# Kernel tuning notes

Hardware: AMD Instinct MI355X
Metric: run time of the kernel (lower is better)

## Reference

```python
import jax, jax.numpy as jnp
import numpy as np

D, NH, NKV, HD, FF, V, T, GEN = 4096, 32, 8, 128, 14336, 1024, 32, 8
ROPE_THETA = 500000.0
EPS = 1e-5


def rms_norm(x, w):
    var = jnp.mean(jnp.square(x), axis=-1, keepdims=True)
    return (x * jax.lax.rsqrt(var + EPS)) * w


def rope_tables(max_pos):
    inv = 1.0 / (ROPE_THETA ** (jnp.arange(0, HD, 2, dtype=jnp.float32) / HD))
    freqs = jnp.arange(max_pos, dtype=jnp.float32)[:, None] * inv[None, :]  # [P, HD/2]
    emb = jnp.concatenate([freqs, freqs], axis=-1)  # [P, HD]
    return jnp.cos(emb), jnp.sin(emb)


def rotate_half(x):
    h = x.shape[-1] // 2
    return jnp.concatenate([-x[..., h:], x[..., :h]], axis=-1)


def setup_inputs() -> dict:
    key = jax.random.key(0)
    ks = jax.random.split(key, 16)
    s = 0.02
    return {
        "chunk_hidden_states": jax.random.normal(ks[0], (1, T, D), jnp.float32),
        "Wq": jax.random.normal(ks[1], (NH * HD, D), jnp.float32) * s,
        "Wk": jax.random.normal(ks[2], (NKV * HD, D), jnp.float32) * s,
        "Wv": jax.random.normal(ks[3], (NKV * HD, D), jnp.float32) * s,
        "Wo": jax.random.normal(ks[4], (D, NH * HD), jnp.float32) * s,
        "w_ln1": jnp.ones((D,), jnp.float32),
        "w_ln2": jnp.ones((D,), jnp.float32),
        "Wg": jax.random.normal(ks[5], (FF, D), jnp.float32) * s,
        "Wu": jax.random.normal(ks[6], (FF, D), jnp.float32) * s,
        "Wd": jax.random.normal(ks[7], (D, FF), jnp.float32) * s,
        "w_norm": jnp.ones((D,), jnp.float32),
        "emb": jax.random.normal(ks[8], (V, D), jnp.float32) * s,
        "W_out": jax.random.normal(ks[9], (V, D), jnp.float32) * s,
        "b_out": jnp.zeros((V,), jnp.float32),
    }


def reference(chunk_hidden_states, Wq, Wk, Wv, Wo, w_ln1, w_ln2, Wg, Wu, Wd,
              w_norm, emb, W_out, b_out):
    # inference=True path: for each of T time steps (processed in parallel here,
    # tokens, re-running the single Llama decoder layer on the growing sequence
    # each step (no KV cache). Only the LAST position's layer output feeds the
    # output head, so we compute q only for the last valid position, which is
    # mathematically identical to the original full-forward + [:, -1, :].
    G = NH // NKV  # query heads per kv head
    x0 = chunk_hidden_states[0]  # [T, D]
    buf = jnp.zeros((T, GEN + 1, D), jnp.float32).at[:, 0].set(x0)
    cos, sin = rope_tables(GEN + 1)  # [GEN+1, HD]
    scale = 1.0 / jnp.sqrt(jnp.float32(HD))

    def step(p, carry):
        buf, toks = carry
        h = rms_norm(buf, w_ln1)  # [T, S, D], S = GEN+1
        k = (h @ Wk.T).reshape(T, GEN + 1, NKV, HD)
        v = (h @ Wv.T).reshape(T, GEN + 1, NKV, HD)
        k = k * cos[None, :, None, :] + rotate_half(k) * sin[None, :, None, :]
        hq = jnp.take(h, p, axis=1)  # [T, D] last valid position
        q = (hq @ Wq.T).reshape(T, NH, HD)
        q = q * cos[p] + rotate_half(q) * sin[p]
        qg = q.reshape(T, NKV, G, HD)
        # scores over keys j (invalid / future keys masked; causal query is pos p)
        scores = jnp.einsum('tgcd,tjgd->tgcj', qg, k) * scale  # [T,NKV,G,S]
        valid = jnp.arange(GEN + 1) <= p
        scores = jnp.where(valid[None, None, None, :], scores, -jnp.inf)
        attn = jax.nn.softmax(scores, axis=-1)
        ao = jnp.einsum('tgcj,tjgd->tgcd', attn, v).reshape(T, NH * HD) @ Wo.T
        xp = jnp.take(buf, p, axis=1) + ao  # attention residual
        h2 = rms_norm(xp, w_ln2)
        mlp = (jax.nn.silu(h2 @ Wg.T) * (h2 @ Wu.T)) @ Wd.T
        xo = xp + mlp  # MLP residual; NOTE: no final norm in inference path
        logits = xo @ W_out.T + b_out  # [T, V]
        tok = jnp.argmax(logits, axis=-1)  # argmax(softmax) == argmax(logits)
        toks = toks.at[:, p].set(tok)
        buf = buf.at[:, p + 1].set(emb[tok])
        return buf, toks

    _, toks = jax.lax.fori_loop(0, GEN, step, (buf, jnp.zeros((T, GEN), jnp.int32)))
    return toks  # [T, 8] predicted tokens
```

## Files before the change

### kernel.cpp

```cpp
#include <hip/hip_runtime.h>
#include <hip/hip_bf16.h>

#define D 4096
#define NH 32
#define NKV 8
#define HD 128
#define FF 14336
#define VOC 1024
#define TT 32
#define GENN 8
#define SEQ 9

#define NQKV 6144
#define NGU  28672

#define OFF_BUF   0ull
#define OFF_KC    1179648ull
#define OFF_VC    1474560ull
#define OFF_AOT   1769472ull
#define OFF_XP    1900544ull
#define OFF_R1    2031616ull
#define OFF_R2    2031680ull
#define OFF_XPK   2031744ull
#define OFF_PART  2490496ull
#define OFF_RED   6684800ull
#define OFF_LR    6881408ull

typedef __attribute__((ext_vector_type(8))) short short8;
typedef __attribute__((ext_vector_type(16))) float f32x16;
typedef __attribute__((address_space(1))) void gv_t;
typedef __attribute__((address_space(3))) void lv_t;

__device__ inline void cvt_hi_lo(const float* x, short8& hi, short8& lo) {
    union U { unsigned u[4]; short8 s; };
    U H, L;
    #pragma unroll
    for (int j = 0; j < 4; ++j) {
        float2 p = make_float2(x[2 * j], x[2 * j + 1]);
        __hip_bfloat162 h = __float22bfloat162_rn(p);
        unsigned hb; __builtin_memcpy(&hb, &h, 4);
        H.u[j] = hb;
        float f0 = __uint_as_float(hb << 16);
        float f1 = __uint_as_float(hb & 0xffff0000u);
        __hip_bfloat162 l = __float22bfloat162_rn(make_float2(p.x - f0, p.y - f1));
        unsigned lb; __builtin_memcpy(&lb, &l, 4);
        L.u[j] = lb;
    }
    hi = H.s; lo = L.s;
}

__device__ inline void store_frag(unsigned* Xp, int frag, int lane,
                                  const short8& hi, const short8& lo) {
    unsigned* dst = Xp + (size_t)frag * 512 + lane * 4;
    union U { short8 s; uint4 u; };
    U uh, ul; uh.s = hi; ul.s = lo;
    *(uint4*)dst = uh.u;
    *(uint4*)(dst + 256) = ul.u;
}

__global__ void k_init(const float* __restrict__ x0, float* __restrict__ buf,
                       float* __restrict__ r1) {
    int t = blockIdx.x;
    const float* src = x0 + (size_t)t * D;
    float* dst = buf + (size_t)t * SEQ * D;
    float ss = 0.f;
    for (int d = threadIdx.x; d < D; d += 256) { float v = src[d]; dst[d] = v; ss += v * v; }
    #pragma unroll
    for (int m = 1; m < 64; m <<= 1) ss += __shfl_xor(ss, m);
    __shared__ float red[4];
    if ((threadIdx.x & 63) == 0) red[threadIdx.x >> 6] = ss;
    __syncthreads();
    if (threadIdx.x == 0) {
        float tot = red[0] + red[1] + red[2] + red[3];
        r1[t] = 1.0f / sqrtf(tot / (float)D + 1e-5f);
    }
}

__global__ void k_rms_rows(const float* __restrict__ x, float* __restrict__ r) {
    int t = blockIdx.x;
    const float* row = x + (size_t)t * D;
    float ss = 0.f;
    for (int d = threadIdx.x; d < D; d += 256) { float v = row[d]; ss += v * v; }
    #pragma unroll
    for (int m = 1; m < 64; m <<= 1) ss += __shfl_xor(ss, m);
    __shared__ float red[4];
    if ((threadIdx.x & 63) == 0) red[threadIdx.x >> 6] = ss;
    __syncthreads();
    if (threadIdx.x == 0) {
        float tot = red[0] + red[1] + red[2] + red[3];
        r[t] = 1.0f / sqrtf(tot / (float)D + 1e-5f);
    }
}

__global__ __launch_bounds__(256) void k_pack_norm(const float* __restrict__ src0,
        int rowStride, const float* __restrict__ r, const float* __restrict__ w,
        unsigned* __restrict__ Xp) {
    int frag = blockIdx.x * 4 + (threadIdx.x >> 6);
    int lane = threadIdx.x & 63;
    int m = lane & 31, half = lane >> 5;
    int k0 = frag * 16 + half * 8;
    const float* src = src0 + (size_t)m * rowStride + k0;
    float rr = r[m];
    float x[8];
    #pragma unroll
    for (int e = 0; e < 8; ++e) x[e] = src[e] * rr * w[k0 + e];
    short8 hi, lo; cvt_hi_lo(x, hi, lo); store_frag(Xp, frag, lane, hi, lo);
}

__global__ __launch_bounds__(256) void k_pack(const float* __restrict__ XT,
                                              unsigned* __restrict__ Xp) {
    int frag = blockIdx.x * 4 + (threadIdx.x >> 6);
    int lane = threadIdx.x & 63;
    int m = lane & 31, half = lane >> 5;
    const float* src = XT + (size_t)(frag * 16 + half * 8) * TT + m;
    float x[8];
    #pragma unroll
    for (int e = 0; e < 8; ++e) x[e] = src[e * TT];
    short8 hi, lo; cvt_hi_lo(x, hi, lo); store_frag(Xp, frag, lane, hi, lo);
}

__global__ __launch_bounds__(256, 2) void k_gemm3(
        const unsigned* __restrict__ Xp, const float* __restrict__ W0,
        const float* __restrict__ W1, const float* __restrict__ W2,
        int t1, int t2, float* __restrict__ part,
        int Nfull, int K, int ntiles, int kc) {
    __shared__ char smem[3 * 20480];
    int wave = threadIdx.x >> 6, lane = threadIdx.x & 63;
    int tile = blockIdx.x % ntiles, split = blockIdx.x / ntiles;
    int k0 = split * kc;
    int m = lane & 31, half = lane >> 5;
    const float* Wsel; int rt;
    if (tile < t1)      { Wsel = W0; rt = tile; }
    else if (tile < t2) { Wsel = W1; rt = tile - t1; }
    else                { Wsel = W2; rt = tile - t2; }
    int r8 = lane >> 3;
    int s8 = lane & 7;
    const float* wsrc = Wsel + (size_t)(rt * 128 + wave * 32 + r8) * K + k0 + ((s8 ^ r8) << 2);
    const unsigned* xsrc = Xp + ((size_t)(k0 >> 4) + (wave >> 1)) * 512 + (wave & 1) * 256 + lane * 4;
    int nph = kc >> 5;

    auto stagef = [&](int ph) {
        char* buf = smem + (ph % 3) * 20480;
        const float* wsp = wsrc + (size_t)ph * 32;
        char* wdb = buf + wave * 4096;
        #pragma unroll
        for (int q = 0; q < 4; ++q) {
            __builtin_amdgcn_global_load_lds(
                (gv_t*)(wsp + (size_t)(q * 8) * K),
                (lv_t*)(wdb + q * 1024), 16, 0, 0);
        }
        __builtin_amdgcn_global_load_lds(
            (gv_t*)(xsrc + (size_t)ph * 1024),
            (lv_t*)(buf + 16384 + wave * 1024), 16, 0, 0);
    };

    f32x16 acc;
    #pragma unroll
    for (int i = 0; i < 16; ++i) acc[i] = 0.f;

    stagef(0);
    if (nph > 1) stagef(1);
    union U { uint4 u; short8 s; };
    for (int ph = 0; ph < nph; ++ph) {
        if (ph + 1 < nph) { asm volatile("s_waitcnt vmcnt(5)" ::: "memory"); }
        else              { asm volatile("s_waitcnt vmcnt(0)" ::: "memory"); }
        __builtin_amdgcn_sched_barrier(0);
        __syncthreads();
        const char* buf = smem + (ph % 3) * 20480;
        const char* wrow = buf + (wave * 32 + m) * 128;
        const char* xb = buf + 16384;
        #pragma unroll
        for (int st = 0; st < 2; ++st) {
            int t0 = st * 4 + half * 2;
            float4 wa = *(const float4*)(wrow + ((t0 ^ (m & 7)) << 4));
            float4 wb = *(const float4*)(wrow + (((t0 + 1) ^ (m & 7)) << 4));
            float xv[8] = {wa.x, wa.y, wa.z, wa.w, wb.x, wb.y, wb.z, wb.w};
            short8 whi, wlo;
            cvt_hi_lo(xv, whi, wlo);
            U bh, bl;
            bh.u = *(const uint4*)(xb + st * 2048 + lane * 16);
            bl.u = *(const uint4*)(xb + st * 2048 + 1024 + lane * 16);
            acc = __builtin_amdgcn_mfma_f32_32x32x16_bf16(whi, bh.s, acc, 0, 0, 0);
            acc = __builtin_amdgcn_mfma_f32_32x32x16_bf16(whi, bl.s, acc, 0, 0, 0);
            acc = __builtin_amdgcn_mfma_f32_32x32x16_bf16(wlo, bh.s, acc, 0, 0, 0);
        }
        if (ph + 2 < nph) stagef(ph + 2);
    }
    int n0 = tile * 128 + wave * 32;
    float* dst = part + (size_t)split * Nfull * TT + (size_t)n0 * TT + m;
    #pragma unroll
    for (int r = 0; r < 16; ++r) {
        int rr = (r & 3) + 8 * (r >> 2) + 4 * half;
        dst[(size_t)rr * TT] = acc[r];
    }
}

__global__ void k_reduce_qkv(const float* __restrict__ part, float* __restrict__ red,
                             int S) {
    int idx = blockIdx.x * 256 + threadIdx.x;
    float a = 0.f;
    for (int s = 0; s < S; ++s) a += part[(size_t)s * NQKV * TT + idx];
    red[idx] = a;
}

__global__ __launch_bounds__(64) void k_attn_f(const float* __restrict__ red,
        float* __restrict__ kcache, float* __restrict__ vcache,
        float* __restrict__ aoT, int p) {
    int t = blockIdx.x >> 5, h = blockIdx.x & 31, kvh = h >> 2;
    int d = threadIdx.x;
    float a  = red[(size_t)(h * HD + d) * TT + t];
    float b  = red[(size_t)(h * HD + d + 64) * TT + t];
    float ak = red[(size_t)(4096 + kvh * HD + d) * TT + t];
    float bk = red[(size_t)(4096 + kvh * HD + d + 64) * TT + t];
    float v0 = red[(size_t)(5120 + kvh * HD + d) * TT + t];
    float v1 = red[(size_t)(5120 + kvh * HD + d + 64) * TT + t];
    float fp = (float)p;
    float ang = fp * powf(500000.0f, -(float)d * (1.0f / 64.0f));
    float cs = cosf(ang), sn = sinf(ang);
    float q0 = a * cs - b * sn,  q1 = b * cs + a * sn;
    float k0r = ak * cs - bk * sn, k1r = bk * cs + ak * sn;
    if ((h & 3) == 0) {
        float* krow = kcache + (((size_t)t * SEQ + p) * NKV + kvh) * HD;
        krow[d] = k0r; krow[d + 64] = k1r;
        float* vrow = vcache + (((size_t)t * SEQ + p) * NKV + kvh) * HD;
        vrow[d] = v0; vrow[d + 64] = v1;
    }
    const float scale = 0.08838834764831845f;
    float sc[SEQ];
    float mx = -1e30f;
    #pragma unroll
    for (int j = 0; j < SEQ; ++j) {
        int jj = (j < p) ? j : p;
        float k0j, k1j;
        if (jj == p) { k0j = k0r; k1j = k1r; }
        else {
            const float* kr = kcache + (((size_t)t * SEQ + jj) * NKV + kvh) * HD;
            k0j = kr[d]; k1j = kr[d + 64];
        }
        float ps = q0 * k0j + q1 * k1j;
        #pragma unroll
        for (int mm = 1; mm < 64; mm <<= 1) ps += __shfl_xor(ps, mm);
        ps = (j <= p) ? ps * scale : -1e30f;
        sc[j] = ps;
        mx = fmaxf(mx, ps);
    }
    float denom = 0.f;
    #pragma unroll
    for (int j = 0; j < SEQ; ++j) {
        float e = expf(sc[j] - mx);
        e = (j <= p) ? e : 0.f;
        sc[j] = e; denom += e;
    }
    float inv = 1.0f / denom;
    float o0 = 0.f, o1 = 0.f;
    #pragma unroll
    for (int j = 0; j < SEQ; ++j) {
        int jj = (j < p) ? j : p;
        float vv0, vv1;
        if (jj == p) { vv0 = v0; vv1 = v1; }
        else {
            const float* vr = vcache + (((size_t)t * SEQ + jj) * NKV + kvh) * HD;
            vv0 = vr[d]; vv1 = vr[d + 64];
        }
        float w = sc[j] * inv;
        o0 = fmaf(w, vv0, o0);
        o1 = fmaf(w, vv1, o1);
    }
    aoT[(size_t)(h * HD + d) * TT + t] = o0;
    aoT[(size_t)(h * HD + d + 64) * TT + t] = o1;
}

__global__ void k_reduce_o(const float* __restrict__ part, const float* __restrict__ buf,
                           float* __restrict__ xp, int p, int S) {
    int idx = blockIdx.x * 256 + threadIdx.x;
    int n = idx >> 5, t = idx & 31;
    float a = 0.f;
    for (int s = 0; s < S; ++s) a += part[(size_t)s * D * TT + idx];
    xp[(size_t)t * D + n] = a + buf[((size_t)t * SEQ + p) * D + n];
}

__global__ __launch_bounds__(256) void k_silu_pack(const float* __restrict__ part,
        unsigned* __restrict__ Xp, int S) {
    int frag = blockIdx.x * 4 + (threadIdx.x >> 6);
    int lane = threadIdx.x & 63;
    int m = lane & 31, half = lane >> 5;
    int n0 = frag * 16 + half * 8;
    float x[8];
    #pragma unroll
    for (int e = 0; e < 8; ++e) {
        int n = n0 + e;
        float g = 0.f, u = 0.f;
        for (int s = 0; s < S; ++s) {
            const float* pb = part + (size_t)s * NGU * TT;
            g += pb[(size_t)n * TT + m];
            u += pb[(size_t)(n + FF) * TT + m];
        }
        float sg = g / (1.0f + expf(-g));
        x[e] = sg * u;
    }
    short8 hi, lo; cvt_hi_lo(x, hi, lo); store_frag(Xp, frag, lane, hi, lo);
}

__global__ __launch_bounds__(256) void k_reduced_pack(const float* __restrict__ part,
        const float* __restrict__ xp, unsigned* __restrict__ Xp, int S) {
    int frag = blockIdx.x * 4 + (threadIdx.x >> 6);
    int lane = threadIdx.x & 63;
    int m = lane & 31, half = lane >> 5;
    int n0 = frag * 16 + half * 8;
    float x[8];
    #pragma unroll
    for (int e = 0; e < 8; ++e) {
        int n = n0 + e;
        float a = 0.f;
        for (int s = 0; s < S; ++s)
            a += part[(size_t)s * D * TT + (size_t)n * TT + m];
        x[e] = a + xp[(size_t)m * D + n];
    }
    short8 hi, lo; cvt_hi_lo(x, hi, lo); store_frag(Xp, frag, lane, hi, lo);
}

__global__ void k_logits_reduce(const float* __restrict__ part,
                                const float* __restrict__ bias,
                                float* __restrict__ lr, int S) {
    int idx = blockIdx.x * 256 + threadIdx.x;
    int n = idx >> 5;
    float a = bias[n];
    for (int s = 0; s < S; ++s) a += part[(size_t)s * VOC * TT + idx];
    lr[idx] = a;
}

__global__ void k_head(const float* __restrict__ lr, const float* __restrict__ emb,
                       int* __restrict__ toks, float* __restrict__ buf,
                       float* __restrict__ r1, int p) {
    int t = blockIdx.x;
    int tid = threadIdx.x;
    float bv = -1e30f; int bi = 0;
    for (int n = tid; n < VOC; n += 256) {
        float a = lr[(size_t)n * TT + t];
        if (a > bv) { bv = a; bi = n; }
    }
    __shared__ float sv[256];
    __shared__ int si[256];
    sv[tid] = bv; si[tid] = bi;
    __syncthreads();
    for (int off = 128; off > 0; off >>= 1) {
        if (tid < off) {
            float v2 = sv[tid + off]; int i2 = si[tid + off];
            if (v2 > sv[tid] || (v2 == sv[tid] && i2 < si[tid])) { sv[tid] = v2; si[tid] = i2; }
        }
        __syncthreads();
    }
    int tok = si[0];
    if (tid == 0) toks[t * GENN + p] = tok;
    const float* er = emb + (size_t)tok * D;
    float* brow = buf + ((size_t)t * SEQ + (p + 1)) * D;
    float ss = 0.f;
    for (int d = tid; d < D; d += 256) { float v = er[d]; brow[d] = v; ss += v * v; }
    #pragma unroll
    for (int m = 1; m < 64; m <<= 1) ss += __shfl_xor(ss, m);
    __shared__ float red[4];
    if ((tid & 63) == 0) red[tid >> 6] = ss;
    __syncthreads();
    if (tid == 0) {
        float tot = red[0] + red[1] + red[2] + red[3];
        r1[t] = 1.0f / sqrtf(tot / (float)D + 1e-5f);
    }
}

extern "C" void kernel_launch(void* const* d_in, const int* in_sizes, int n_in,
                              void* d_out, int out_size, void* d_ws, size_t ws_size,
                              hipStream_t stream) {
    const float* x0   = (const float*)d_in[0];
    const float* Wq   = (const float*)d_in[1];
    const float* Wk   = (const float*)d_in[2];
    const float* Wv   = (const float*)d_in[3];
    const float* Wo   = (const float*)d_in[4];
    const float* wln1 = (const float*)d_in[5];
    const float* wln2 = (const float*)d_in[6];
    const float* Wg   = (const float*)d_in[7];
    const float* Wu   = (const float*)d_in[8];
    const float* Wd   = (const float*)d_in[9];
    const float* emb  = (const float*)d_in[11];
    const float* Wout = (const float*)d_in[12];
    const float* bout = (const float*)d_in[13];

    float* ws   = (float*)d_ws;
    float* buf  = ws + OFF_BUF;
    float* kcc  = ws + OFF_KC;
    float* vcc  = ws + OFF_VC;
    float* aoT  = ws + OFF_AOT;
    float* xp   = ws + OFF_XP;
    float* r1   = ws + OFF_R1;
    float* r2   = ws + OFF_R2;
    unsigned* Xpk = (unsigned*)(ws + OFF_XPK);
    float* part = ws + OFF_PART;
    float* redq = ws + OFF_RED;
    float* lr   = ws + OFF_LR;

    size_t availF = (ws_size / 4 > OFF_PART) ? (4194304) : 0;
    auto fitS = [&](int smax, size_t cols, int K) {
        int s = smax;
        while (s > 1 && (size_t)s * cols * TT > availF) s >>= 1;
        while (s > 1 && (((K / s) % 32) || (K / s) < 64)) s >>= 1;
        return s;
    };
    const int S_qkv = fitS(16, NQKV, D);
    const int S_wo  = fitS(16, D, D);
    const int S_gu  = fitS(4,  NGU, D);
    const int S_wd  = fitS(16, D, FF);
    const int S_out = fitS(64, VOC, D);
    const int kc_qkv = D / S_qkv;
    const int kc_wo  = D / S_wo;
    const int kc_gu  = D / S_gu;
    const int kc_wd  = FF / S_wd;
    const int kc_out = D / S_out;
    const int BIG = 1 << 20;

    k_init<<<32, 256, 0, stream>>>(x0, buf, r1);
    for (int p = 0; p < GENN; ++p) {
        k_pack_norm<<<64, 256, 0, stream>>>(buf + (size_t)p * D, SEQ * D, r1, wln1, Xpk);
        k_gemm3<<<48 * S_qkv, 256, 0, stream>>>(Xpk, Wq, Wk, Wv, 32, 40,
                                                part, NQKV, D, 48, kc_qkv);
        k_reduce_qkv<<<NQKV * TT / 256, 256, 0, stream>>>(part, redq, S_qkv);
        k_attn_f<<<1024, 64, 0, stream>>>(redq, kcc, vcc, aoT, p);
        k_pack<<<64, 256, 0, stream>>>(aoT, Xpk);
        k_gemm3<<<32 * S_wo, 256, 0, stream>>>(Xpk, Wo, Wo, Wo, BIG, BIG,
                                               part, D, D, 32, kc_wo);
        k_reduce_o<<<512, 256, 0, stream>>>(part, buf, xp, p, S_wo);
        k_rms_rows<<<32, 256, 0, stream>>>(xp, r2);
        k_pack_norm<<<64, 256, 0, stream>>>(xp, D, r2, wln2, Xpk);
        k_gemm3<<<224 * S_gu, 256, 0, stream>>>(Xpk, Wg, Wu, Wu, 112, BIG,
                                                part, NGU, D, 224, kc_gu);
        k_silu_pack<<<224, 256, 0, stream>>>(part, Xpk, S_gu);
        k_gemm3<<<32 * S_wd, 256, 0, stream>>>(Xpk, Wd, Wd, Wd, BIG, BIG,
                                               part, D, FF, 32, kc_wd);
        k_reduced_pack<<<64, 256, 0, stream>>>(part, xp, Xpk, S_wd);
        k_gemm3<<<8 * S_out, 256, 0, stream>>>(Xpk, Wout, Wout, Wout, BIG, BIG,
                                               part, VOC, D, 8, kc_out);
        k_logits_reduce<<<VOC * TT / 256, 256, 0, stream>>>(part, bout, lr, S_out);
        k_head<<<32, 256, 0, stream>>>(lr, emb, (int*)d_out, buf, r1, p);
    }
}
```

Baseline: 2.543 ms.

## Pre-pack fp32 weights into bf16 hi/lo MFMA fragment layout

Adds a per-call weight packing pass that converts every fp32 weight matrix into bf16 hi/lo split fragments, stored contiguously in the exact per-block, per-phase order the GEMM consumes. A new GEMM kernel then streams these packed tiles with simple contiguous loads into LDS, removing strided row loads and the per-step fp32-to-bf16 split conversion across the 8 decode steps. The cost is an extra full read and write of all weights every call, plus a very large workspace requirement. If the workspace is too small, the code falls back to the old path.

```diff
diff --git a/kernel.cpp b/kernel.cpp
--- a/kernel.cpp
+++ b/kernel.cpp
@@ -25,6 +25,13 @@
 #define OFF_PART  2490496ull
 #define OFF_RED   6684800ull
 #define OFF_LR    6881408ull
+#define OFF_PACK  6914176ull
+#define PK_QKV 0ull
+#define PK_WO  25165824ull
+#define PK_GU  41943040ull
+#define PK_WD  159383552ull
+#define PK_OUT 218103808ull
+#define PK_TOTAL 222298112ull
 
 typedef __attribute__((ext_vector_type(8))) short short8;
 typedef __attribute__((ext_vector_type(16))) float f32x16;
@@ -117,6 +124,105 @@
     #pragma unroll
     for (int e = 0; e < 8; ++e) x[e] = src[e * TT];
     short8 hi, lo; cvt_hi_lo(x, hi, lo); store_frag(Xp, frag, lane, hi, lo);
+}
+
+__global__ __launch_bounds__(256) void k_pack_w(const float* __restrict__ W,
+        unsigned* __restrict__ dst, int K, int kc, int nph, int ntiles,
+        int rowsBase, int nRowTiles) {
+    int b = blockIdx.x;
+    int ph = b % nph; int rest = b / nph;
+    int tLoc = rest % nRowTiles; int s = rest / nRowTiles;
+    int kbase = s * kc + ph * 32;
+    __shared__ float lds[128][33];
+    int t = threadIdx.x;
+    int r = t >> 1, c0 = (t & 1) * 16;
+    const float* src = W + (size_t)(tLoc * 128 + r) * K + kbase + c0;
+    #pragma unroll
+    for (int j = 0; j < 16; j += 4) {
+        float4 v = *(const float4*)(src + j);
+        lds[r][c0 + j] = v.x; lds[r][c0 + j + 1] = v.y;
+        lds[r][c0 + j + 2] = v.z; lds[r][c0 + j + 3] = v.w;
+    }
+    __syncthreads();
+    size_t blk = (size_t)s * ntiles + rowsBase + tLoc;
+    #pragma unroll
+    for (int fid = t; fid < 512; fid += 256) {
+        int lane = fid & 63, step = (fid >> 6) & 1, wv = fid >> 7;
+        int m = lane & 31, half = lane >> 5;
+        int row = wv * 32 + m;
+        int kl = step * 16 + half * 8;
+        float x[8];
+        #pragma unroll
+        for (int e = 0; e < 8; ++e) x[e] = lds[row][kl + e];
+        short8 hi, lo; cvt_hi_lo(x, hi, lo);
+        unsigned* d0 = dst + (blk * nph + ph) * 4096 + wv * 1024 + step * 512 + lane * 4;
+        union U { short8 s; uint4 u; };
+        U uh, ul; uh.s = hi; ul.s = lo;
+        *(uint4*)d0 = uh.u;
+        *(uint4*)(d0 + 256) = ul.u;
+    }
+}
+
+__global__ __launch_bounds__(256, 2) void k_gemmP(
+        const unsigned* __restrict__ Xp, const unsigned* __restrict__ pk,
+        float* __restrict__ part, int Nfull, int ntiles, int kc) {
+    __shared__ char smem[3 * 20480];
+    int wave = threadIdx.x >> 6, lane = threadIdx.x & 63;
+    int tile = blockIdx.x % ntiles, split = blockIdx.x / ntiles;
+    int k0 = split * kc;
+    int m = lane & 31, half = lane >> 5;
+    int nph = kc >> 5;
+    const char* wbase = (const char*)pk + (size_t)blockIdx.x * nph * 16384
+                        + wave * 4096 + lane * 16;
+    const unsigned* xsrc = Xp + ((size_t)(k0 >> 4) + (wave >> 1)) * 512 + (wave & 1) * 256 + lane * 4;
+
+    auto stagef = [&](int ph) {
+        char* buf = smem + (ph % 3) * 20480;
+        const char* wsp = wbase + (size_t)ph * 16384;
+        char* wdb = buf + wave * 4096;
+        #pragma unroll
+        for (int q = 0; q < 4; ++q)
+            __builtin_amdgcn_global_load_lds((gv_t*)(wsp + q * 1024),
+                                             (lv_t*)(wdb + q * 1024), 16, 0, 0);
+        __builtin_amdgcn_global_load_lds((gv_t*)(xsrc + (size_t)ph * 1024),
+                                         (lv_t*)(buf + 16384 + wave * 1024), 16, 0, 0);
+    };
+
+    f32x16 acc;
+    #pragma unroll
+    for (int i = 0; i < 16; ++i) acc[i] = 0.f;
+
+    stagef(0);
+    if (nph > 1) stagef(1);
+    union U { uint4 u; short8 s; };
+    for (int ph = 0; ph < nph; ++ph) {
+        if (ph + 1 < nph) { asm volatile("s_waitcnt vmcnt(5)" ::: "memory"); }
+        else              { asm volatile("s_waitcnt vmcnt(0)" ::: "memory"); }
+        __builtin_amdgcn_sched_barrier(0);
+        __syncthreads();
+        const char* buf = smem + (ph % 3) * 20480;
+        const char* wb = buf + wave * 4096;
+        const char* xb = buf + 16384;
+        #pragma unroll
+        for (int st = 0; st < 2; ++st) {
+            U ah, al, bh, bl;
+            ah.u = *(const uint4*)(wb + st * 2048 + lane * 16);
+            al.u = *(const uint4*)(wb + st * 2048 + 1024 + lane * 16);
+            bh.u = *(const uint4*)(xb + st * 2048 + lane * 16);
+            bl.u = *(const uint4*)(xb + st * 2048 + 1024 + lane * 16);
+            acc = __builtin_amdgcn_mfma_f32_32x32x16_bf16(ah.s, bh.s, acc, 0, 0, 0);
+            acc = __builtin_amdgcn_mfma_f32_32x32x16_bf16(ah.s, bl.s, acc, 0, 0, 0);
+            acc = __builtin_amdgcn_mfma_f32_32x32x16_bf16(al.s, bh.s, acc, 0, 0, 0);
+        }
+        if (ph + 2 < nph) stagef(ph + 2);
+    }
+    int n0 = tile * 128 + wave * 32;
+    float* dst = part + (size_t)split * Nfull * TT + (size_t)n0 * TT + m;
+    #pragma unroll
+    for (int r = 0; r < 16; ++r) {
+        int rr = (r & 3) + 8 * (r >> 2) + 4 * half;
+        dst[(size_t)rr * TT] = acc[r];
+    }
 }
 
 __global__ __launch_bounds__(256, 2) void k_gemm3(
@@ -144,14 +250,11 @@
         const float* wsp = wsrc + (size_t)ph * 32;
         char* wdb = buf + wave * 4096;
         #pragma unroll
-        for (int q = 0; q < 4; ++q) {
-            __builtin_amdgcn_global_load_lds(
-                (gv_t*)(wsp + (size_t)(q * 8) * K),
-                (lv_t*)(wdb + q * 1024), 16, 0, 0);
-        }
-        __builtin_amdgcn_global_load_lds(
-            (gv_t*)(xsrc + (size_t)ph * 1024),
-            (lv_t*)(buf + 16384 + wave * 1024), 16, 0, 0);
+        for (int q = 0; q < 4; ++q)
+            __builtin_amdgcn_global_load_lds((gv_t*)(wsp + (size_t)(q * 8) * K),
+                                             (lv_t*)(wdb + q * 1024), 16, 0, 0);
+        __builtin_amdgcn_global_load_lds((gv_t*)(xsrc + (size_t)ph * 1024),
+                                         (lv_t*)(buf + 16384 + wave * 1024), 16, 0, 0);
     };
 
     f32x16 acc;
@@ -396,8 +499,11 @@
     float* part = ws + OFF_PART;
     float* redq = ws + OFF_RED;
     float* lr   = ws + OFF_LR;
-
-    size_t availF = (ws_size / 4 > OFF_PART) ? (4194304) : 0;
+    unsigned* pk = (unsigned*)(ws + OFF_PACK);
+
+    const bool packed = (ws_size / 4) >= (OFF_PACK + PK_TOTAL);
+
+    size_t availF = 4194304;
     auto fitS = [&](int smax, size_t cols, int K) {
         int s = smax;
         while (s > 1 && (size_t)s * cols * TT > availF) s >>= 1;
@@ -416,27 +522,53 @@
     const int kc_out = D / S_out;
     const int BIG = 1 << 20;
 
+    if (packed) {
+        k_pack_w<<<S_qkv * 32 * (kc_qkv / 32), 256, 0, stream>>>(Wq, pk + PK_QKV, D, kc_qkv, kc_qkv / 32, 48, 0, 32);
+        k_pack_w<<<S_qkv * 8  * (kc_qkv / 32), 256, 0, stream>>>(Wk, pk + PK_QKV, D, kc_qkv, kc_qkv / 32, 48, 32, 8);
+        k_pack_w<<<S_qkv * 8  * (kc_qkv / 32), 256, 0, stream>>>(Wv, pk + PK_QKV, D, kc_qkv, kc_qkv / 32, 48, 40, 8);
+        k_pack_w<<<S_wo * 32 * (kc_wo / 32), 256, 0, stream>>>(Wo, pk + PK_WO, D, kc_wo, kc_wo / 32, 32, 0, 32);
+        k_pack_w<<<S_gu * 112 * (kc_gu / 32), 256, 0, stream>>>(Wg, pk + PK_GU, D, kc_gu, kc_gu / 32, 224, 0, 112);
+        k_pack_w<<<S_gu * 112 * (kc_gu / 32), 256, 0, stream>>>(Wu, pk + PK_GU, D, kc_gu, kc_gu / 32, 224, 112, 112);
+        k_pack_w<<<S_wd * 32 * (kc_wd / 32), 256, 0, stream>>>(Wd, pk + PK_WD, FF, kc_wd, kc_wd / 32, 32, 0, 32);
+        k_pack_w<<<S_out * 8 * (kc_out / 32), 256, 0, stream>>>(Wout, pk + PK_OUT, D, kc_out, kc_out / 32, 8, 0, 8);
+    }
+
     k_init<<<32, 256, 0, stream>>>(x0, buf, r1);
     for (int p = 0; p < GENN; ++p) {
         k_pack_norm<<<64, 256, 0, stream>>>(buf + (size_t)p * D, SEQ * D, r1, wln1, Xpk);
-        k_gemm3<<<48 * S_qkv, 256, 0, stream>>>(Xpk, Wq, Wk, Wv, 32, 40,
-                                                part, NQKV, D, 48, kc_qkv);
+        if (packed)
+            k_gemmP<<<48 * S_qkv, 256, 0, stream>>>(Xpk, pk + PK_QKV, part, NQKV, 48, kc_qkv);
+        else
+            k_gemm3<<<48 * S_qkv, 256, 0, stream>>>(Xpk, Wq, Wk, Wv, 32, 40,
+                                                    part, NQKV, D, 48, kc_qkv);
         k_reduce_qkv<<<NQKV * TT / 256, 256, 0, stream>>>(part, redq, S_qkv);
         k_attn_f<<<1024, 64, 0, stream>>>(redq, kcc, vcc, aoT, p);
         k_pack<<<64, 256, 0, stream>>>(aoT, Xpk);
-        k_gemm3<<<32 * S_wo, 256, 0, stream>>>(Xpk, Wo, Wo, Wo, BIG, BIG,
-                                               part, D, D, 32, kc_wo);
+        if (packed)
+            k_gemmP<<<32 * S_wo, 256, 0, stream>>>(Xpk, pk + PK_WO, part, D, 32, kc_wo);
+        else
+            k_gemm3<<<32 * S_wo, 256, 0, stream>>>(Xpk, Wo, Wo, Wo, BIG, BIG,
+                                                   part, D, D, 32, kc_wo);
         k_reduce_o<<<512, 256, 0, stream>>>(part, buf, xp, p, S_wo);
         k_rms_rows<<<32, 256, 0, stream>>>(xp, r2);
         k_pack_norm<<<64, 256, 0, stream>>>(xp, D, r2, wln2, Xpk);
-        k_gemm3<<<224 * S_gu, 256, 0, stream>>>(Xpk, Wg, Wu, Wu, 112, BIG,
-                                                part, NGU, D, 224, kc_gu);
+        if (packed)
+            k_gemmP<<<224 * S_gu, 256, 0, stream>>>(Xpk, pk + PK_GU, part, NGU, 224, kc_gu);
+        else
+            k_gemm3<<<224 * S_gu, 256, 0, stream>>>(Xpk, Wg, Wu, Wu, 112, BIG,
+                                                    part, NGU, D, 224, kc_gu);
         k_silu_pack<<<224, 256, 0, stream>>>(part, Xpk, S_gu);
-        k_gemm3<<<32 * S_wd, 256, 0, stream>>>(Xpk, Wd, Wd, Wd, BIG, BIG,
-                                               part, D, FF, 32, kc_wd);
+        if (packed)
+            k_gemmP<<<32 * S_wd, 256, 0, stream>>>(Xpk, pk + PK_WD, part, D, 32, kc_wd);
+        else
+            k_gemm3<<<32 * S_wd, 256, 0, stream>>>(Xpk, Wd, Wd, Wd, BIG, BIG,
+                                                   part, D, FF, 32, kc_wd);
         k_reduced_pack<<<64, 256, 0, stream>>>(part, xp, Xpk, S_wd);
-        k_gemm3<<<8 * S_out, 256, 0, stream>>>(Xpk, Wout, Wout, Wout, BIG, BIG,
-                                               part, VOC, D, 8, kc_out);
+        if (packed)
+            k_gemmP<<<8 * S_out, 256, 0, stream>>>(Xpk, pk + PK_OUT, part, VOC, 8, kc_out);
+        else
+            k_gemm3<<<8 * S_out, 256, 0, stream>>>(Xpk, Wout, Wout, Wout, BIG, BIG,
+                                                   part, VOC, D, 8, kc_out);
         k_logits_reduce<<<VOC * TT / 256, 256, 0, stream>>>(part, bout, lr, S_out);
         k_head<<<32, 256, 0, stream>>>(lr, emb, (int*)d_out, buf, r1, p);
     }
```

New measurement: 2.687 ms. 5.7% more time.
